# Kernel tuning notes

Measured on AMD Instinct MI355X. Metric: run time of the kernel, lower is better.

Reference implementation:

```python
import jax, jax.numpy as jnp
import numpy as np

B, T, D = 2, 512, 512
NUM_SCALES, MIN_S, MAX_S = 10, 0.01, 1.0
SCALES_NP = np.logspace(np.log10(MIN_S), np.log10(MAX_S), NUM_SCALES)


def _golay():
    # extended Golay (24,12) generator exactly as in _initialize_golay_code
    G = np.zeros((12, 24), np.float32)
    for i in range(12):
        G[i, i] = 1.0
        for j in range(11):
            G[i, 12 + j] = (i + j) % 2
        G[i, 23] = G[i, :23].sum() % 2
    return jnp.asarray(G)

GOLAY = _golay()  # [12,24]


def setup_inputs() -> dict:
    key = jax.random.key(0)
    ks = jax.random.split(key, 6)
    return {
        'token_ids': jax.random.randint(ks[0], (B, T), 0, 1000000, dtype=jnp.int32),
        'resonances': jax.random.uniform(ks[1], (D,), minval=1.0, maxval=50.0, dtype=jnp.float32),
        'emb_scales': jnp.ones((D,), jnp.float32),
        'emb_shifts': jnp.zeros((D,), jnp.float32),
        'emb_norm': jnp.ones((1,), jnp.float32),
        'scale_weights': jnp.ones((NUM_SCALES,), jnp.float32),
        'fractal_bias': jnp.zeros((1,), jnp.float32),
        'frac_norm': jnp.ones((1,), jnp.float32),
        'W_enc': jax.random.normal(ks[2], (D, 24), jnp.float32) / np.float32(np.sqrt(D)),
        'b_enc': jnp.zeros((24,), jnp.float32),
        'W_dec': jax.random.normal(ks[3], (24, D), jnp.float32) / np.float32(np.sqrt(24)),
        'b_dec': jnp.zeros((D,), jnp.float32),
        'ecc_strength': jnp.full((1,), 0.1, jnp.float32),
        'energy_preservation': jnp.ones((1,), jnp.float32),
    }


def _fractal_dimension(signal, scale_weights, fractal_bias, frac_norm):
    # differentiable box-counting (GenuineFractalAnalyzer.compute_fractal_dimension)
    input_energy = jnp.linalg.norm(signal)
    s = signal.reshape(-1)  # [N]
    s = (s - s.min()) / (s.max() - s.min() + 1e-8)
    counts = []
    for scale_np in SCALES_NP:
        nb = int(round(1.0 / scale_np))  # static per scale: 100 ... 1
        edges = jnp.linspace(0.0, 1.0, nb + 1)
        lo, hi = edges[:-1][:, None], edges[1:][:, None]  # [nb,1]
        # vectorized over boxes instead of python loop over boxes
        in_box = jax.nn.sigmoid(10.0 * (s[None, :] - lo)) * jax.nn.sigmoid(10.0 * (hi - s[None, :]))  # [nb,N]
        occ = in_box.sum(axis=1)  # [nb]
        counts.append(jax.nn.sigmoid(occ - 0.5).sum())
    box_counts = jnp.stack(counts)  # [NUM_SCALES]
    weighted = box_counts * jax.nn.softmax(scale_weights)
    scales = jnp.asarray(SCALES_NP, jnp.float32)
    log_x = jnp.log(1.0 / scales)
    log_y = jnp.log(weighted + 1e-8)
    n = np.float32(NUM_SCALES)
    sx, sy = log_x.sum(), log_y.sum()
    sxy, sx2 = (log_x * log_y).sum(), (log_x ** 2).sum()
    slope = (n * sxy - sx * sy) / (n * sx2 - sx ** 2 + 1e-8)
    fd = jnp.clip(-slope + fractal_bias, 1.0, 2.5)  # [1]
    out_energy = jnp.linalg.norm(fd)
    return fd * frac_norm * input_energy / out_energy


def reference(token_ids, resonances, emb_scales, emb_shifts, emb_norm, scale_weights,
              fractal_bias, frac_norm, W_enc, b_enc, W_dec, b_dec, ecc_strength,
              energy_preservation):
    # --- GenuineEmbedding.batch_encode (vectorized over B,T,D) ---
    token_value = (token_ids % 1000000).astype(jnp.float32) / 1e6  # [B,T]
    pos = jnp.arange(T, dtype=jnp.float32)  # [T]
    angle = resonances[None, None, :] * (token_value[:, :, None] + pos[None, :, None])  # [B,T,D]
    c, sn = jnp.cos(angle), jnp.sin(angle)
    comp = c * (1.0 + sn) + sn * sn
    emb = comp * emb_scales + emb_shifts
    tok_norm = jnp.linalg.norm(emb, axis=-1, keepdims=True)
    emb = jnp.where(tok_norm > 0, emb * emb_norm / tok_norm, emb)

    # --- GenuineLeechLattice.encode_to_lattice ---
    ecc = ecc_strength[0]
    ep = energy_preservation[0]
    e_in = jnp.linalg.norm(emb, axis=-1, keepdims=True)  # b t 1
    proj = emb @ W_enc + b_enc  # [B,T,24]
    golay_enc = jnp.einsum('btl,kl->btk', proj, GOLAY)  # [B,T,12]
    latt = jnp.round(golay_enc / ecc) * ecc
    e_out = jnp.linalg.norm(latt, axis=-1, keepdims=True)
    latt = latt * (e_in / (e_out + 1e-8)) * ep

    # --- GenuineLeechLattice.decode_from_lattice ---
    e_in2 = jnp.linalg.norm(latt, axis=-1, keepdims=True)
    golay_dec = jnp.einsum('btk,kl->btl', latt, GOLAY)  # [B,T,24]
    corrected = jnp.where(jnp.abs(golay_dec) > ecc, golay_dec, 0.0)
    res = corrected @ W_dec + b_dec  # [B,T,D]
    e_out2 = jnp.linalg.norm(res, axis=-1, keepdims=True)
    res = res * (e_in2 / (e_out2 + 1e-8)) * ep

    # --- GenuineFractalAnalyzer on the corrected signal, then modulate ---
    fd = _fractal_dimension(res, scale_weights, fractal_bias, frac_norm)  # [1]
    return res * fd
```

## Files before the change

### kernel.cpp

```cpp
#include <hip/hip_runtime.h>
#include <math.h>

#define NT   1024
#define TT   512
#define DD   512


__device__ __forceinline__ float np_pairwise512(const float* x, int tid) {
    float r = 0.0f;
    if (tid < 32) {
        const int b = tid >> 3, j = tid & 7;
        const float* p = x + 128 * b + j;
        r = p[0];
        #pragma unroll
        for (int i = 1; i < 16; i++) r = __fadd_rn(r, p[8 * i]);
    }
    r = __fadd_rn(r, __shfl_down(r, 1, 64));
    r = __fadd_rn(r, __shfl_down(r, 2, 64));
    r = __fadd_rn(r, __shfl_down(r, 4, 64));
    r = __fadd_rn(r, __shfl_down(r, 8, 64));
    r = __fadd_rn(r, __shfl_down(r, 16, 64));
    return r;
}

__device__ __forceinline__ float np_pairwise12(const float* a) {
    float r = __fadd_rn(__fadd_rn(__fadd_rn(a[0], a[1]), __fadd_rn(a[2], a[3])),
                        __fadd_rn(__fadd_rn(a[4], a[5]), __fadd_rn(a[6], a[7])));
    r = __fadd_rn(r, a[8]);
    r = __fadd_rn(r, a[9]);
    r = __fadd_rn(r, a[10]);
    r = __fadd_rn(r, a[11]);
    return r;
}

__global__ __launch_bounds__(256) void token_kernel(
    const int*   __restrict__ token_ids,
    const float* __restrict__ resonances,
    const float* __restrict__ emb_scales,
    const float* __restrict__ emb_shifts,
    const float* __restrict__ emb_norm,
    const float* __restrict__ W_enc,
    const float* __restrict__ b_enc,
    const float* __restrict__ W_dec,
    const float* __restrict__ b_dec,
    const float* __restrict__ ecc_p,
    const float* __restrict__ ep_p,
    float*       __restrict__ out,
    double*      __restrict__ partials)
{
    const int tok  = blockIdx.x;
    const int t    = tok % TT;
    const int tid  = threadIdx.x;
    const int lane = tid & 63;
    const int wave = tid >> 6;

    __shared__ float  sh_e[DD];
    __shared__ float  sh_x[DD];
    __shared__ float  sh_p[24];
    __shared__ float  sh_c[24];
    __shared__ float  sh_l[12];
    __shared__ float  sh_sc[4];
    __shared__ double sh_red[4];

    const float ecc   = ecc_p[0];
    const float ep    = ep_p[0];
    const float enorm = emb_norm[0];

    const int   idv  = token_ids[tok];
    const float tv   = __fdiv_rn((float)idv, 1000000.0f);
    const float base = __fadd_rn(tv, (float)t);

    const int d0 = tid, d1 = tid + 256;
    float e0, e1;
    {
        const float a0 = __fmul_rn(resonances[d0], base);
        const float a1 = __fmul_rn(resonances[d1], base);
        double s0d, c0d, s1d, c1d;
        sincos((double)a0, &s0d, &c0d);
        sincos((double)a1, &s1d, &c1d);
        const float s0 = (float)s0d, c0 = (float)c0d;
        const float s1 = (float)s1d, c1 = (float)c1d;
        const float comp0 = __fadd_rn(__fmul_rn(c0, __fadd_rn(1.0f, s0)), __fmul_rn(s0, s0));
        const float comp1 = __fadd_rn(__fmul_rn(c1, __fadd_rn(1.0f, s1)), __fmul_rn(s1, s1));
        e0 = __fadd_rn(__fmul_rn(comp0, emb_scales[d0]), emb_shifts[d0]);
        e1 = __fadd_rn(__fmul_rn(comp1, emb_scales[d1]), emb_shifts[d1]);
    }
    sh_x[d0] = __fmul_rn(e0, e0);
    sh_x[d1] = __fmul_rn(e1, e1);
    __syncthreads();

    float ps = np_pairwise512(sh_x, tid);
    if (tid == 0) sh_sc[0] = __fsqrt_rn(ps);
    __syncthreads();
    const float tok_norm = sh_sc[0];
    if (tok_norm > 0.0f) {
        e0 = __fdiv_rn(__fmul_rn(e0, enorm), tok_norm);
        e1 = __fdiv_rn(__fmul_rn(e1, enorm), tok_norm);
    }
    sh_e[d0] = e0; sh_e[d1] = e1;
    sh_x[d0] = __fmul_rn(e0, e0);
    sh_x[d1] = __fmul_rn(e1, e1);
    __syncthreads();

    ps = np_pairwise512(sh_x, tid);
    const float e_in = __fsqrt_rn(ps);
    __syncthreads();

    if (tid < 24) {
        float acc = 0.0f;
        #pragma unroll 8
        for (int d = 0; d < DD; d++)
            acc = fmaf(sh_e[d], W_enc[d * 24 + tid], acc);
        sh_p[tid] = __fadd_rn(acc, b_enc[tid]);
    }
    __syncthreads();

    if (tid < 12) {
        const int k = tid;
        float g = sh_p[k];
        #pragma unroll
        for (int l = 12; l < 23; l++)
            if ((k + l) & 1) g = __fadd_rn(g, sh_p[l]);
        if (k & 1) g = __fadd_rn(g, sh_p[23]);
        sh_l[k] = __fmul_rn(rintf(__fdiv_rn(g, ecc)), ecc);
    }
    __syncthreads();

    if (tid == 0) {
        float sq[12];
        #pragma unroll
        for (int k = 0; k < 12; k++) sq[k] = __fmul_rn(sh_l[k], sh_l[k]);
        const float e_out = __fsqrt_rn(np_pairwise12(sq));
        const float m1 = __fdiv_rn(e_in, __fadd_rn(e_out, 1e-8f));
        #pragma unroll
        for (int k = 0; k < 12; k++) {
            const float lv = __fmul_rn(__fmul_rn(sh_l[k], m1), ep);
            sh_l[k] = lv;
            sq[k] = __fmul_rn(lv, lv);
        }
        sh_sc[2] = __fsqrt_rn(np_pairwise12(sq));
    }
    __syncthreads();

    if (tid < 24) {
        const int l = tid;
        float g;
        if (l < 12) {
            g = sh_l[l];
        } else if (l < 23) {
            g = 0.0f;
            #pragma unroll
            for (int k = 0; k < 12; k++)
                if ((k + l) & 1) g = __fadd_rn(g, sh_l[k]);
        } else {
            g = 0.0f;
            for (int k = 1; k < 12; k += 2) g = __fadd_rn(g, sh_l[k]);
        }
        sh_c[l] = (fabsf(g) > ecc) ? g : 0.0f;
    }
    __syncthreads();

    float r0 = 0.0f, r1 = 0.0f;
    #pragma unroll
    for (int l = 0; l < 24; l++) {
        const float cl = sh_c[l];
        r0 = fmaf(cl, W_dec[l * DD + d0], r0);
        r1 = fmaf(cl, W_dec[l * DD + d1], r1);
    }
    r0 = __fadd_rn(r0, b_dec[d0]);
    r1 = __fadd_rn(r1, b_dec[d1]);
    sh_x[d0] = __fmul_rn(r0, r0);
    sh_x[d1] = __fmul_rn(r1, r1);
    __syncthreads();
    ps = np_pairwise512(sh_x, tid);
    if (tid == 0) sh_sc[3] = __fsqrt_rn(ps);
    __syncthreads();

    const float m2 = __fdiv_rn(sh_sc[2], __fadd_rn(sh_sc[3], 1e-8f));
    const float f0 = __fmul_rn(__fmul_rn(r0, m2), ep);
    const float f1 = __fmul_rn(__fmul_rn(r1, m2), ep);
    out[tok * DD + d0] = f0;
    out[tok * DD + d1] = f1;

    double v4 = (double)f0 * (double)f0 + (double)f1 * (double)f1;
    for (int off = 32; off > 0; off >>= 1) v4 += __shfl_down(v4, off, 64);
    if (lane == 0) sh_red[wave] = v4;
    __syncthreads();
    if (tid == 0) partials[tok] = sh_red[0] + sh_red[1] + sh_red[2] + sh_red[3];
}

__global__ __launch_bounds__(256) void reduce_kernel(
    const double* __restrict__ partials,
    const float*  __restrict__ frac_norm,
    float*        __restrict__ factor_out)
{
    const int tid = threadIdx.x;
    __shared__ double sh[4];
    double s = 0.0;
    #pragma unroll
    for (int i = 0; i < 4; i++) s += partials[tid + 256 * i];
    for (int off = 32; off > 0; off >>= 1) s += __shfl_down(s, off, 64);
    if ((tid & 63) == 0) sh[tid >> 6] = s;
    __syncthreads();
    if (tid == 0)
        factor_out[0] = (float)((double)frac_norm[0] * sqrt(sh[0] + sh[1] + sh[2] + sh[3]));
}

__global__ __launch_bounds__(256) void scale_kernel(
    float* __restrict__ out,
    const float* __restrict__ factor_p)
{
    const int i = blockIdx.x * blockDim.x + threadIdx.x;
    const float factor = factor_p[0];
    float4 r = ((const float4*)out)[i];
    r.x = __fmul_rn(r.x, factor);
    r.y = __fmul_rn(r.y, factor);
    r.z = __fmul_rn(r.z, factor);
    r.w = __fmul_rn(r.w, factor);
    ((float4*)out)[i] = r;
}

extern "C" void kernel_launch(void* const* d_in, const int* in_sizes, int n_in,
                              void* d_out, int out_size, void* d_ws, size_t ws_size,
                              hipStream_t stream)
{
    const int*   token_ids  = (const int*)  d_in[0];
    const float* resonances = (const float*)d_in[1];
    const float* emb_scales = (const float*)d_in[2];
    const float* emb_shifts = (const float*)d_in[3];
    const float* emb_norm   = (const float*)d_in[4];
    const float* frac_norm  = (const float*)d_in[7];
    const float* W_enc      = (const float*)d_in[8];
    const float* b_enc      = (const float*)d_in[9];
    const float* W_dec      = (const float*)d_in[10];
    const float* b_dec      = (const float*)d_in[11];
    const float* ecc        = (const float*)d_in[12];
    const float* ep         = (const float*)d_in[13];

    double* partials = (double*)d_ws;
    float*  factor   = (float*)((char*)d_ws + NT * sizeof(double));

    token_kernel<<<NT, 256, 0, stream>>>(token_ids, resonances, emb_scales, emb_shifts,
                                         emb_norm, W_enc, b_enc, W_dec, b_dec, ecc, ep,
                                         (float*)d_out, partials);
    reduce_kernel<<<1, 256, 0, stream>>>(partials, frac_norm, factor);
    scale_kernel<<<(NT * DD) / 1024, 256, 0, stream>>>((float*)d_out, factor);
}
```

Baseline: 105.9 us.

## Use one thread per element in token kernel and fuse reduce into scale kernel

The token kernel now runs 512 threads per block, so each thread handles one embedding element instead of two, with 8-wave reduction slots. The separate single-block reduce kernel is removed: every scale block redundantly sums the 1024 per-token partials and computes the factor in shared memory before scaling its slice. This drops one kernel launch and serial dependency and raises the number of threads available to hide the double-precision sincos latency. In exchange, every scale block repeats the partial reduction, and larger blocks may reduce occupancy.

```diff
diff --git a/kernel.cpp b/kernel.cpp
--- a/kernel.cpp
+++ b/kernel.cpp
@@ -33,7 +33,7 @@
     return r;
 }
 
-__global__ __launch_bounds__(256) void token_kernel(
+__global__ __launch_bounds__(512, 8) void token_kernel(
     const int*   __restrict__ token_ids,
     const float* __restrict__ resonances,
     const float* __restrict__ emb_scales,
@@ -60,7 +60,7 @@
     __shared__ float  sh_c[24];
     __shared__ float  sh_l[12];
     __shared__ float  sh_sc[4];
-    __shared__ double sh_red[4];
+    __shared__ double sh_red[8];
 
     const float ecc   = ecc_p[0];
     const float ep    = ep_p[0];
@@ -70,36 +70,26 @@
     const float tv   = __fdiv_rn((float)idv, 1000000.0f);
     const float base = __fadd_rn(tv, (float)t);
 
-    const int d0 = tid, d1 = tid + 256;
-    float e0, e1;
+    float e0;
     {
-        const float a0 = __fmul_rn(resonances[d0], base);
-        const float a1 = __fmul_rn(resonances[d1], base);
-        double s0d, c0d, s1d, c1d;
+        const float a0 = __fmul_rn(resonances[tid], base);
+        double s0d, c0d;
         sincos((double)a0, &s0d, &c0d);
-        sincos((double)a1, &s1d, &c1d);
         const float s0 = (float)s0d, c0 = (float)c0d;
-        const float s1 = (float)s1d, c1 = (float)c1d;
         const float comp0 = __fadd_rn(__fmul_rn(c0, __fadd_rn(1.0f, s0)), __fmul_rn(s0, s0));
-        const float comp1 = __fadd_rn(__fmul_rn(c1, __fadd_rn(1.0f, s1)), __fmul_rn(s1, s1));
-        e0 = __fadd_rn(__fmul_rn(comp0, emb_scales[d0]), emb_shifts[d0]);
-        e1 = __fadd_rn(__fmul_rn(comp1, emb_scales[d1]), emb_shifts[d1]);
-    }
-    sh_x[d0] = __fmul_rn(e0, e0);
-    sh_x[d1] = __fmul_rn(e1, e1);
+        e0 = __fadd_rn(__fmul_rn(comp0, emb_scales[tid]), emb_shifts[tid]);
+    }
+    sh_x[tid] = __fmul_rn(e0, e0);
     __syncthreads();
 
     float ps = np_pairwise512(sh_x, tid);
     if (tid == 0) sh_sc[0] = __fsqrt_rn(ps);
     __syncthreads();
     const float tok_norm = sh_sc[0];
-    if (tok_norm > 0.0f) {
+    if (tok_norm > 0.0f)
         e0 = __fdiv_rn(__fmul_rn(e0, enorm), tok_norm);
-        e1 = __fdiv_rn(__fmul_rn(e1, enorm), tok_norm);
-    }
-    sh_e[d0] = e0; sh_e[d1] = e1;
-    sh_x[d0] = __fmul_rn(e0, e0);
-    sh_x[d1] = __fmul_rn(e1, e1);
+    sh_e[tid] = e0;
+    sh_x[tid] = __fmul_rn(e0, e0);
     __syncthreads();
 
     ps = np_pairwise512(sh_x, tid);
@@ -160,17 +150,12 @@
     }
     __syncthreads();
 
-    float r0 = 0.0f, r1 = 0.0f;
+    float r0 = 0.0f;
     #pragma unroll
-    for (int l = 0; l < 24; l++) {
-        const float cl = sh_c[l];
-        r0 = fmaf(cl, W_dec[l * DD + d0], r0);
-        r1 = fmaf(cl, W_dec[l * DD + d1], r1);
-    }
-    r0 = __fadd_rn(r0, b_dec[d0]);
-    r1 = __fadd_rn(r1, b_dec[d1]);
-    sh_x[d0] = __fmul_rn(r0, r0);
-    sh_x[d1] = __fmul_rn(r1, r1);
+    for (int l = 0; l < 24; l++)
+        r0 = fmaf(sh_c[l], W_dec[l * DD + tid], r0);
+    r0 = __fadd_rn(r0, b_dec[tid]);
+    sh_x[tid] = __fmul_rn(r0, r0);
     __syncthreads();
     ps = np_pairwise512(sh_x, tid);
     if (tid == 0) sh_sc[3] = __fsqrt_rn(ps);
@@ -178,24 +163,28 @@
 
     const float m2 = __fdiv_rn(sh_sc[2], __fadd_rn(sh_sc[3], 1e-8f));
     const float f0 = __fmul_rn(__fmul_rn(r0, m2), ep);
-    const float f1 = __fmul_rn(__fmul_rn(r1, m2), ep);
-    out[tok * DD + d0] = f0;
-    out[tok * DD + d1] = f1;
-
-    double v4 = (double)f0 * (double)f0 + (double)f1 * (double)f1;
+    out[tok * DD + tid] = f0;
+
+    double v4 = (double)f0 * (double)f0;
     for (int off = 32; off > 0; off >>= 1) v4 += __shfl_down(v4, off, 64);
     if (lane == 0) sh_red[wave] = v4;
     __syncthreads();
-    if (tid == 0) partials[tok] = sh_red[0] + sh_red[1] + sh_red[2] + sh_red[3];
-}
-
-__global__ __launch_bounds__(256) void reduce_kernel(
+    if (tid == 0) {
+        double s = sh_red[0];
+        #pragma unroll
+        for (int w = 1; w < 8; w++) s += sh_red[w];
+        partials[tok] = s;
+    }
+}
+
+__global__ __launch_bounds__(256) void scale_kernel(
+    float*        __restrict__ out,
     const double* __restrict__ partials,
-    const float*  __restrict__ frac_norm,
-    float*        __restrict__ factor_out)
+    const float*  __restrict__ frac_norm)
 {
     const int tid = threadIdx.x;
     __shared__ double sh[4];
+    __shared__ float sh_factor;
     double s = 0.0;
     #pragma unroll
     for (int i = 0; i < 4; i++) s += partials[tid + 256 * i];
@@ -203,15 +192,11 @@
     if ((tid & 63) == 0) sh[tid >> 6] = s;
     __syncthreads();
     if (tid == 0)
-        factor_out[0] = (float)((double)frac_norm[0] * sqrt(sh[0] + sh[1] + sh[2] + sh[3]));
-}
-
-__global__ __launch_bounds__(256) void scale_kernel(
-    float* __restrict__ out,
-    const float* __restrict__ factor_p)
-{
-    const int i = blockIdx.x * blockDim.x + threadIdx.x;
-    const float factor = factor_p[0];
+        sh_factor = (float)((double)frac_norm[0] * sqrt(sh[0] + sh[1] + sh[2] + sh[3]));
+    __syncthreads();
+    const float factor = sh_factor;
+
+    const int i = blockIdx.x * blockDim.x + tid;
     float4 r = ((const float4*)out)[i];
     r.x = __fmul_rn(r.x, factor);
     r.y = __fmul_rn(r.y, factor);
@@ -238,11 +223,9 @@
     const float* ep         = (const float*)d_in[13];
 
     double* partials = (double*)d_ws;
-    float*  factor   = (float*)((char*)d_ws + NT * sizeof(double));
-
-    token_kernel<<<NT, 256, 0, stream>>>(token_ids, resonances, emb_scales, emb_shifts,
+
+    token_kernel<<<NT, 512, 0, stream>>>(token_ids, resonances, emb_scales, emb_shifts,
                                          emb_norm, W_enc, b_enc, W_dec, b_dec, ecc, ep,
                                          (float*)d_out, partials);
-    reduce_kernel<<<1, 256, 0, stream>>>(partials, frac_norm, factor);
-    scale_kernel<<<(NT * DD) / 1024, 256, 0, stream>>>((float*)d_out, factor);
-}
+    scale_kernel<<<(NT * DD) / 1024, 256, 0, stream>>>((float*)d_out, partials, frac_norm);
+}
```

After: 105.3 us. No clear change (-0.5%).
